# Kernel optimization log

Measured on AMD Instinct MI355X. Metric: run time of the kernel, lower is better.

## Reference

```python
import jax, jax.numpy as jnp
import numpy as np

ABS_DIM, HIDDEN, ACTION_DIM, N_TASKS, B = 512, 512, 18, 16, 8192
W_SCALE = 0.001


def setup_inputs() -> dict:
    key = jax.random.key(0)
    k1, k2, k3, k4, k5 = jax.random.split(key, 5)
    x = jax.random.normal(k1, (B, ABS_DIM), dtype=jnp.float32)
    task_id = jax.random.randint(k2, (B,), 0, N_TASKS)
    action = jax.random.randint(k3, (B,), 0, ACTION_DIM)
    # Per-task weight banks (MultiLinear), w_scale=0.001
    W1 = jax.random.normal(k4, (N_TASKS, ABS_DIM, HIDDEN), dtype=jnp.float32) * W_SCALE
    b1 = jnp.zeros((N_TASKS, HIDDEN), dtype=jnp.float32)
    W2 = jax.random.normal(k5, (N_TASKS, HIDDEN, ACTION_DIM), dtype=jnp.float32) * W_SCALE
    b2 = jnp.zeros((N_TASKS, ACTION_DIM), dtype=jnp.float32)
    return {"x": x, "task_id": task_id, "action": action,
            "W1": W1, "b1": b1, "W2": W2, "b2": b2}


def _multi_linear(x, W, b, task_id):
    # x: [B, din], W: [T, din, dout], b: [T, dout]
    # Compute all experts then select per-sample (dense grouped-GEMM form).
    y_all = jnp.einsum('bi,tio->tbo', x, W) + b[:, None, :]  # [T, B, dout]
    rows = jnp.arange(x.shape[0])
    return y_all[task_id, rows]  # [B, dout]


def reference(x, task_id, action, W1, b1, W2, b2):
    h = jax.nn.relu(_multi_linear(x, W1, b1, task_id))          # [B, H]
    logits = _multi_linear(h, W2, b2, task_id)                  # [B, A]
    logprobs = jax.nn.log_softmax(logits, axis=1)               # [B, A]
    rows = jnp.arange(x.shape[0])
    log_pi_a = logprobs[rows, action][:, None]                  # [B, 1]
    ent = -jnp.sum(jnp.exp(logprobs) * logprobs, axis=1, keepdims=True)  # [B, 1]
    # forward output: concat of log_pi_a and entropy (action passes through)
    return jnp.concatenate([log_pi_a, ent], axis=1)             # [B, 2]
```

## Files before the change

kernel.cpp:

```cpp
#include <hip/hip_runtime.h>
#include <hip/hip_bf16.h>

#define B_N   8192
#define DIN   512
#define DH    512
#define NACT  18
#define NTASK 16
#define BM    64
#define BN    64
#define BK    32
#define PJ    20
#define NSLOT 1280
#define SPILL 256

typedef __attribute__((ext_vector_type(8))) short  short8v;
typedef __attribute__((ext_vector_type(8))) unsigned short ushort8v;
typedef __attribute__((ext_vector_type(4))) unsigned short ushort4v;
typedef __attribute__((ext_vector_type(4))) float  float4v;
typedef __attribute__((ext_vector_type(2))) float  float2v;

typedef const __attribute__((address_space(1))) void* gas_ptr;
typedef __attribute__((address_space(3))) void* las_ptr;

__device__ __forceinline__ unsigned short f2bf(float f) {
  union { float f; unsigned int u; } c; c.f = f;
  unsigned int u = c.u;
  u += 0x7fffu + ((u >> 16) & 1u);
  return (unsigned short)(u >> 16);
}

__global__ __launch_bounds__(256) void k_pre(
    const float* __restrict__ W2, const int* __restrict__ task_id,
    short* __restrict__ W2T, int* __restrict__ tbl, int* __restrict__ rowidx) {
  __shared__ float ldsB[64 * 19];
  __shared__ int c4[4][NTASK], cur4[4][NTASK];
  int bx = blockIdx.x, tid = threadIdx.x;

  if (bx == 0) {
    if (tid < 64) ((int*)c4)[tid] = 0;
    __syncthreads();
    for (int i = tid; i < B_N; i += 256)
      atomicAdd(&c4[i >> 11][task_id[i]], 1);
    __syncthreads();
    if (tid == 0) {
      int acc = 0;
#pragma unroll
      for (int t = 0; t < NTASK; ++t) {
        int c = c4[0][t] + c4[1][t] + c4[2][t] + c4[3][t];
        tbl[t] = c; tbl[16 + t] = acc;
        int o = acc;
#pragma unroll
        for (int q = 0; q < 4; ++q) { cur4[q][t] = o; o += c4[q][t]; }
        acc += c;
      }
    }
    __syncthreads();
    for (int i = tid; i < B_N; i += 256) {
      int t = task_id[i];
      rowidx[atomicAdd(&cur4[i >> 11][t], 1)] = i;
    }
  } else {
    int u = bx - 1;
    int t = u >> 3, k0 = (u & 7) * 64;
    for (int i = tid; i < 64 * NACT; i += 256) {
      int kk = i / NACT, j = i - kk * NACT;
      ldsB[kk * 19 + j] = W2[((size_t)t * DIN + k0 + kk) * NACT + j];
    }
    __syncthreads();
    for (int o = tid; o < 32 * 64; o += 256) {
      int j = o >> 6, kk = o & 63;
      float val = (j < NACT) ? ldsB[kk * 19 + j] : 0.0f;
      W2T[((size_t)t * 32 + j) * DIN + k0 + kk] = (short)f2bf(val);
    }
  }
}

__global__ __launch_bounds__(256, 5) void k_gemm1(
    const float* __restrict__ x, const float* __restrict__ bias1,
    const float* __restrict__ W1, const short* __restrict__ W2Tg,
    const int* __restrict__ tbl, const int* __restrict__ rowidx,
    float* __restrict__ pbuf) {
  __shared__ __align__(16) short sA[2][BM * 40];
  __shared__ __align__(16) short sB[2][BN * 40];
  short* sH  = sA[0];
  short* sW2 = sB[0];
  __shared__ int s_rows[64];
  int tid = threadIdx.x, lane = tid & 63, wave = tid >> 6;

  int b = blockIdx.x;
  int t = -1, rel = 0;
  if (b < NSLOT) {
    int r = b & 7, q = b >> 3;
    int n0t = (tbl[r] + 63) >> 6, n1t = (tbl[r + 8] + 63) >> 6;
    if (q < 8 * n0t) { t = r; rel = q; }
    else if (q < 8 * (n0t + n1t)) { t = r + 8; rel = q - 8 * n0t; }
    else return;
  } else {
    int j = b - NSLOT;
    for (int r = 0; r < 8; ++r) {
      int n0t = (tbl[r] + 63) >> 6, n1t = (tbl[r + 8] + 63) >> 6;
      int P = 8 * (n0t + n1t);
      int S = (P > 160) ? (P - 160) : 0;
      if (j < S) {
        int q = 160 + j;
        if (q < 8 * n0t) { t = r; rel = q; }
        else { t = r + 8; rel = q - 8 * n0t; }
        break;
      }
      j -= S;
    }
    if (t < 0) return;
  }
  int itile = rel >> 3, cs = rel & 7;
  int cnt_t = tbl[t], off_t = tbl[16 + t];
  int row0 = off_t + itile * 64;
  int mcnt = cnt_t - itile * 64; if (mcnt > 64) mcnt = 64;
  int n0 = cs * BN;

  if (tid < 64) {
    int idx = row0 + tid;
    if (idx > B_N - 1) idx = B_N - 1;
    s_rows[tid] = rowidx[idx];
  }
  __syncthreads();

  int arow = tid >> 2, ak8 = (tid & 3) << 3;
  const float* xrow = x + (size_t)s_rows[arow] * DIN + ak8;
  int bh = tid >> 7, bkq = (tid >> 4) & 7, bnq = tid & 15;
  int bn = bnq * 4 + bh * 2;
  const float* w1b = W1 + ((size_t)t * DIN + bkq * 4) * DH + n0 + bn;

  float4v La0, La1;
  float2v Lb0, Lb1, Lb2, Lb3;
#define LOAD_A(k0e) {                                                        \
    const float* xs_ = xrow + (k0e);                                         \
    La0 = *(const float4v*)xs_;                                              \
    La1 = *(const float4v*)(xs_ + 4); }
#define WRITE_A(buf) {                                                       \
    ushort8v p0;                                                             \
    _Pragma("unroll") for (int i_ = 0; i_ < 4; ++i_) {                       \
      p0[i_] = f2bf(La0[i_]); p0[4 + i_] = f2bf(La1[i_]); }                  \
    *(ushort8v*)&sA[buf][arow * 40 + ak8] = p0; }
#define LOAD_B(k0e) {                                                        \
    const float* wb_ = w1b + (size_t)(k0e) * DH;                             \
    Lb0 = *(const float2v*)(wb_);                                            \
    Lb1 = *(const float2v*)(wb_ + DH);                                       \
    Lb2 = *(const float2v*)(wb_ + 2 * DH);                                   \
    Lb3 = *(const float2v*)(wb_ + 3 * DH); }
#define WRITE_B(buf) {                                                       \
    _Pragma("unroll") for (int c_ = 0; c_ < 2; ++c_) {                       \
      ushort4v pk;                                                           \
      pk[0] = f2bf(Lb0[c_]); pk[1] = f2bf(Lb1[c_]);                          \
      pk[2] = f2bf(Lb2[c_]); pk[3] = f2bf(Lb3[c_]);                          \
      *(ushort4v*)&sB[buf][(bn + c_) * 40 + bkq * 4] = pk; } }

  LOAD_A(0)
  LOAD_B(0)
  WRITE_A(0)
  WRITE_B(0)
  __syncthreads();

  float4v acc[4];
#pragma unroll
  for (int i = 0; i < 4; ++i) acc[i] = (float4v)0.0f;

#pragma unroll
  for (int step = 0; step < 16; ++step) {
    const int p = step & 1;
    if (step < 15) {
      LOAD_A((step + 1) * BK)
      LOAD_B((step + 1) * BK)
    }
    short8v a, bfr[4];
    {
      int r = wave * 16 + (lane & 15);
      a = *(const short8v*)&sA[p][r * 40 + ((lane >> 4) << 3)];
    }
#pragma unroll
    for (int fn = 0; fn < 4; ++fn) {
      int r = fn * 16 + (lane & 15);
      bfr[fn] = *(const short8v*)&sB[p][r * 40 + ((lane >> 4) << 3)];
    }
#pragma unroll
    for (int fn = 0; fn < 4; ++fn)
      acc[fn] = __builtin_amdgcn_mfma_f32_16x16x32_bf16(a, bfr[fn], acc[fn], 0, 0, 0);
    if (step < 15) {
      WRITE_A(p ^ 1)
      WRITE_B(p ^ 1)
    }
    __syncthreads();
  }

#pragma unroll
  for (int fn = 0; fn < 4; ++fn) {
    int n = fn * 16 + (lane & 15);
    float bias = bias1[t * DH + n0 + n];
#pragma unroll
    for (int r = 0; r < 4; ++r) {
      int m = wave * 16 + ((lane >> 4) << 2) + r;
      float v = fmaxf(acc[fn][r] + bias, 0.0f);
      *(short*)((char*)sH + m * 128 + (((n >> 3) ^ (m & 7)) << 4) + ((n & 7) << 1)) =
          (short)f2bf(v);
    }
  }
  {
    int j = tid >> 3, c2 = tid & 7;
    ushort8v w = *(const ushort8v*)(W2Tg + ((size_t)t * 32 + j) * DIN + n0 + c2 * 8);
    *(ushort8v*)&sW2[(j * 8 + (c2 ^ (j & 7))) * 8] = w;
  }
  __syncthreads();

  float4v acc2[2];
  acc2[0] = (float4v)0.0f; acc2[1] = (float4v)0.0f;
#pragma unroll
  for (int ks = 0; ks < 2; ++ks) {
    int mrow = wave * 16 + (lane & 15);
    int ca = (ks * 4 + (lane >> 4)) ^ (mrow & 7);
    short8v af = *(const short8v*)((char*)sH + mrow * 128 + (ca << 4));
#pragma unroll
    for (int fn = 0; fn < 2; ++fn) {
      int j = fn * 16 + (lane & 15);
      int cb = (ks * 4 + (lane >> 4)) ^ (j & 7);
      short8v bf = *(const short8v*)&sW2[(j * 8 + cb) * 8];
      acc2[fn] = __builtin_amdgcn_mfma_f32_16x16x32_bf16(af, bf, acc2[fn], 0, 0, 0);
    }
  }
#pragma unroll
  for (int fn = 0; fn < 2; ++fn) {
#pragma unroll
    for (int r = 0; r < 4; ++r) {
      int m = wave * 16 + ((lane >> 4) << 2) + r;
      int j = fn * 16 + (lane & 15);
      if (m < mcnt && j < PJ)
        pbuf[((size_t)cs * B_N + row0 + m) * PJ + j] = acc2[fn][r];
    }
  }
#undef LOAD_A
#undef WRITE_A
#undef LOAD_B
#undef WRITE_B
}

__global__ __launch_bounds__(256) void k_soft(
    const float* __restrict__ pbuf, const float* __restrict__ bias2,
    const int* __restrict__ task_id, const int* __restrict__ action,
    const int* __restrict__ rowidx, float* __restrict__ out) {
  __shared__ float acc[256 * PJ];
  int tid = threadIdx.x;
  int base = blockIdx.x * 256;
#pragma unroll
  for (int it = 0; it < 5; ++it) {
    int idx = it * 256 + tid;
    int row = idx / 5, j4 = idx - row * 5;
    float4v s = (float4v)0.0f;
#pragma unroll
    for (int c = 0; c < 8; ++c)
      s += *(const float4v*)&pbuf[((size_t)c * B_N + base + row) * PJ + j4 * 4];
    *(float4v*)&acc[row * PJ + j4 * 4] = s;
  }
  __syncthreads();

  int srow = base + tid;
  int orig = rowidx[srow];
  int t = task_id[orig], act = action[orig];
  float lg[NACT];
#pragma unroll
  for (int j = 0; j < NACT; ++j) lg[j] = acc[tid * PJ + j] + bias2[t * NACT + j];
  float mx = lg[0];
#pragma unroll
  for (int j = 1; j < NACT; ++j) mx = fmaxf(mx, lg[j]);
  float s1 = 0.0f, s2 = 0.0f, la = 0.0f;
#pragma unroll
  for (int j = 0; j < NACT; ++j) {
    float e = __expf(lg[j] - mx);
    s1 += e; s2 += e * lg[j];
    la = (j == act) ? lg[j] : la;
  }
  float logZ = __logf(s1);
  float2v o;
  o[0] = la - mx - logZ;
  o[1] = (mx + logZ) - s2 / s1;
  *(float2v*)(out + (size_t)orig * 2) = o;
}

extern "C" void kernel_launch(void* const* d_in, const int* in_sizes, int n_in,
                              void* d_out, int out_size, void* d_ws, size_t ws_size,
                              hipStream_t stream) {
  const float* x       = (const float*)d_in[0];
  const int*   task_id = (const int*)d_in[1];
  const int*   action  = (const int*)d_in[2];
  const float* W1      = (const float*)d_in[3];
  const float* b1      = (const float*)d_in[4];
  const float* W2      = (const float*)d_in[5];
  const float* b2      = (const float*)d_in[6];
  float* out = (float*)d_out;

  char* ws = (char*)d_ws;
  int* tbl    = (int*)ws;
  int* rowidx = (int*)(ws + 4096);
  size_t off = 36864;
  short* W2T  = (short*)(ws + off);  off += (size_t)NTASK * 32 * DIN * 2;
  float* pbuf = (float*)(ws + off);

  k_pre<<<129, 256, 0, stream>>>(W2, task_id, W2T, tbl, rowidx);
  k_gemm1<<<NSLOT + SPILL, 256, 0, stream>>>(x, b1, W1, W2T, tbl, rowidx, pbuf);
  k_soft<<<32, 256, 0, stream>>>(pbuf, b2, task_id, action, rowidx, out);
}
```

Measured before the change: 48.60 us.

## Stage full W1 column tile in LDS upfront instead of double-buffered K slices

The k_gemm1 kernel now loads the entire 512x64 W1 slice for its task and column block into a 64KB XOR-swizzled LDS buffer before the K loop. The loop then streams only the x tile through double-buffered LDS. This removes the per-step B loads and conversions from the inner loop and issues all W1 loads at once for more memory-level parallelism. In exchange, LDS use grows sharply, launch bounds drop from 5 to 2 blocks per CU, and every block pays a serialized upfront load before any MFMA work starts.

```diff
diff --git a/kernel.cpp b/kernel.cpp
--- a/kernel.cpp
+++ b/kernel.cpp
@@ -19,9 +19,6 @@
 typedef __attribute__((ext_vector_type(4))) float  float4v;
 typedef __attribute__((ext_vector_type(2))) float  float2v;
 
-typedef const __attribute__((address_space(1))) void* gas_ptr;
-typedef __attribute__((address_space(3))) void* las_ptr;
-
 __device__ __forceinline__ unsigned short f2bf(float f) {
   union { float f; unsigned int u; } c; c.f = f;
   unsigned int u = c.u;
@@ -75,15 +72,15 @@
   }
 }
 
-__global__ __launch_bounds__(256, 5) void k_gemm1(
+__global__ __launch_bounds__(256, 2) void k_gemm1(
     const float* __restrict__ x, const float* __restrict__ bias1,
     const float* __restrict__ W1, const short* __restrict__ W2Tg,
     const int* __restrict__ tbl, const int* __restrict__ rowidx,
     float* __restrict__ pbuf) {
+  __shared__ __align__(16) short sBfull[BN * DIN];
   __shared__ __align__(16) short sA[2][BM * 40];
-  __shared__ __align__(16) short sB[2][BN * 40];
   short* sH  = sA[0];
-  short* sW2 = sB[0];
+  short* sW2 = sBfull;
   __shared__ int s_rows[64];
   int tid = threadIdx.x, lane = tid & 63, wave = tid >> 6;
 
@@ -122,16 +119,36 @@
     if (idx > B_N - 1) idx = B_N - 1;
     s_rows[tid] = rowidx[idx];
   }
+
+  {
+    int nc4 = tid & 15, kr4 = tid >> 4;
+    const float* wsrc = W1 + (size_t)t * DIN * DH + n0 + nc4 * 4;
+#pragma unroll
+    for (int kb = 0; kb < 8; ++kb) {
+      int k0 = kb * 64 + kr4 * 4;
+      const float* s_ = wsrc + (size_t)k0 * DH;
+      float4v r0 = *(const float4v*)(s_);
+      float4v r1 = *(const float4v*)(s_ + DH);
+      float4v r2 = *(const float4v*)(s_ + 2 * DH);
+      float4v r3 = *(const float4v*)(s_ + 3 * DH);
+      int cbase = k0 >> 3;
+      int half  = (kr4 & 1) * 8;
+#pragma unroll
+      for (int i = 0; i < 4; ++i) {
+        int n = nc4 * 4 + i;
+        ushort4v pk;
+        pk[0] = f2bf(r0[i]); pk[1] = f2bf(r1[i]);
+        pk[2] = f2bf(r2[i]); pk[3] = f2bf(r3[i]);
+        *(ushort4v*)((char*)sBfull + n * 1024 + ((cbase ^ (n & 7)) << 4) + half) = pk;
+      }
+    }
+  }
+
+  int arow = tid >> 2, ak8 = (tid & 3) << 3;
   __syncthreads();
-
-  int arow = tid >> 2, ak8 = (tid & 3) << 3;
   const float* xrow = x + (size_t)s_rows[arow] * DIN + ak8;
-  int bh = tid >> 7, bkq = (tid >> 4) & 7, bnq = tid & 15;
-  int bn = bnq * 4 + bh * 2;
-  const float* w1b = W1 + ((size_t)t * DIN + bkq * 4) * DH + n0 + bn;
 
   float4v La0, La1;
-  float2v Lb0, Lb1, Lb2, Lb3;
 #define LOAD_A(k0e) {                                                        \
     const float* xs_ = xrow + (k0e);                                         \
     La0 = *(const float4v*)xs_;                                              \
@@ -141,23 +158,9 @@
     _Pragma("unroll") for (int i_ = 0; i_ < 4; ++i_) {                       \
       p0[i_] = f2bf(La0[i_]); p0[4 + i_] = f2bf(La1[i_]); }                  \
     *(ushort8v*)&sA[buf][arow * 40 + ak8] = p0; }
-#define LOAD_B(k0e) {                                                        \
-    const float* wb_ = w1b + (size_t)(k0e) * DH;                             \
-    Lb0 = *(const float2v*)(wb_);                                            \
-    Lb1 = *(const float2v*)(wb_ + DH);                                       \
-    Lb2 = *(const float2v*)(wb_ + 2 * DH);                                   \
-    Lb3 = *(const float2v*)(wb_ + 3 * DH); }
-#define WRITE_B(buf) {                                                       \
-    _Pragma("unroll") for (int c_ = 0; c_ < 2; ++c_) {                       \
-      ushort4v pk;                                                           \
-      pk[0] = f2bf(Lb0[c_]); pk[1] = f2bf(Lb1[c_]);                          \
-      pk[2] = f2bf(Lb2[c_]); pk[3] = f2bf(Lb3[c_]);                          \
-      *(ushort4v*)&sB[buf][(bn + c_) * 40 + bkq * 4] = pk; } }
 
   LOAD_A(0)
-  LOAD_B(0)
   WRITE_A(0)
-  WRITE_B(0)
   __syncthreads();
 
   float4v acc[4];
@@ -169,7 +172,6 @@
     const int p = step & 1;
     if (step < 15) {
       LOAD_A((step + 1) * BK)
-      LOAD_B((step + 1) * BK)
     }
     short8v a, bfr[4];
     {
@@ -179,14 +181,14 @@
 #pragma unroll
     for (int fn = 0; fn < 4; ++fn) {
       int r = fn * 16 + (lane & 15);
-      bfr[fn] = *(const short8v*)&sB[p][r * 40 + ((lane >> 4) << 3)];
+      int c = step * 4 + (lane >> 4);
+      bfr[fn] = *(const short8v*)((char*)sBfull + r * 1024 + ((c ^ (r & 7)) << 4));
     }
 #pragma unroll
     for (int fn = 0; fn < 4; ++fn)
       acc[fn] = __builtin_amdgcn_mfma_f32_16x16x32_bf16(a, bfr[fn], acc[fn], 0, 0, 0);
     if (step < 15) {
       WRITE_A(p ^ 1)
-      WRITE_B(p ^ 1)
     }
     __syncthreads();
   }
@@ -237,8 +239,6 @@
   }
 #undef LOAD_A
 #undef WRITE_A
-#undef LOAD_B
-#undef WRITE_B
 }
 
 __global__ __launch_bounds__(256) void k_soft(
```

After: 59.75 us. 1.23x slower.
